# Performance work log

Hardware: AMD Instinct MI355X
Metric: run time of the kernel (lower is better)

Reference implementation:

```python
import jax, jax.numpy as jnp
import numpy as np

N = 100000      # nodes
E = 3200000     # edges (avg degree 32)
F_IN = 16       # node_features
HID = 32        # hidden_channels
OUT = 1         # out_channels


def _glorot(key, shape, fan_in):
    return (jax.random.normal(key, shape, dtype=jnp.float32) / np.sqrt(fan_in)).astype(jnp.float32)


def setup_inputs() -> dict:
    key = jax.random.key(0)
    ks = jax.random.split(key, 18)
    inp = {
        "x": jax.random.normal(ks[0], (N, F_IN), dtype=jnp.float32),
        "edge_index": jax.random.randint(ks[1], (2, E), 0, N, dtype=jnp.int64),
        "edge_weight": jax.random.uniform(ks[2], (E,), dtype=jnp.float32),
    }
    # 6 ChebConvs (K=2): x->gate convs take F_IN, h->gate convs take HID
    names_in = [("xz", F_IN), ("hz", HID), ("xr", F_IN), ("hr", HID), ("xh", F_IN), ("hh", HID)]
    for i, (nm, fin) in enumerate(names_in):
        inp[f"W_{nm}"] = _glorot(ks[3 + i], (2, fin, HID), fin)   # [K=2, in, hidden]
        inp[f"b_{nm}"] = jnp.zeros((HID,), dtype=jnp.float32)
    inp["W_lin"] = _glorot(ks[15], (HID, OUT), HID)
    inp["b_lin"] = jnp.zeros((OUT,), dtype=jnp.float32)
    return inp


def _cheb(x, W, b, src, dst, lhat_w, n):
    # ChebConv K=2, lambda_max=2: Tx0 = x, Tx1 = L_hat @ x
    tx1 = jax.ops.segment_sum(lhat_w[:, None] * x[src], dst, num_segments=n)
    return x @ W[0] + tx1 @ W[1] + b


def reference(x, edge_index, edge_weight,
              W_xz, b_xz, W_hz, b_hz,
              W_xr, b_xr, W_hr, b_hr,
              W_xh, b_xh, W_hh, b_hh,
              W_lin, b_lin):
    n = x.shape[0]
    src, dst = edge_index[0], edge_index[1]
    # scaled Laplacian edge weights: L_hat = -D^{-1/2} A D^{-1/2} (diag cancels)
    deg = jax.ops.segment_sum(edge_weight, src, num_segments=n)
    dis = jnp.where(deg > 0, jax.lax.rsqrt(jnp.maximum(deg, 1e-12)), 0.0)
    lhat_w = -dis[src] * edge_weight * dis[dst]

    H = jnp.zeros((n, W_hz.shape[1]), dtype=x.dtype)  # initial hidden state

    Z = jax.nn.sigmoid(_cheb(x, W_xz, b_xz, src, dst, lhat_w, n)
                       + _cheb(H, W_hz, b_hz, src, dst, lhat_w, n))
    R = jax.nn.sigmoid(_cheb(x, W_xr, b_xr, src, dst, lhat_w, n)
                       + _cheb(H, W_hr, b_hr, src, dst, lhat_w, n))
    H_tilde = jnp.tanh(_cheb(x, W_xh, b_xh, src, dst, lhat_w, n)
                       + _cheb(H * R, W_hh, b_hh, src, dst, lhat_w, n))
    H_new = Z * H + (1.0 - Z) * H_tilde

    h = jax.nn.relu(H_new)
    return h @ W_lin + b_lin
```

## Files before the change

### kernel.cpp

```cpp
#include <hip/hip_runtime.h>
#include <hip/hip_fp16.h>

#define N_NODES 100000
#define N_EDGES 3200000
#define F_IN 16
#define HID 32

#define NPB 128
#define NBIN 782
#define NBLK_A 512
#define EPB (N_EDGES / NBLK_A)
#define EPB2 (EPB / 2)
#define CAPB 4576
#define CAPT 9
#define SLOTS 7

typedef unsigned long long ull;
typedef float __attribute__((ext_vector_type(4))) f4v;
typedef float __attribute__((ext_vector_type(2))) f2v;

#define OFF_GCA  0
#define OFF_GCB  784
#define OFF_DIS  1568
#define OFF_XSH  101568
#define OFF_EB   901568
#define OFF_EBS  8058432

__device__ inline float2 h2f(unsigned u)
{
    __half2 h = *reinterpret_cast<__half2*>(&u);
    return __half22float2(h);
}

__global__ __launch_bounds__(512) void scatterC(
    const int* __restrict__ src, const int* __restrict__ dst,
    const float* __restrict__ w,
    int* __restrict__ gcurA, int* __restrict__ gcurB,
    uint2* __restrict__ eb, unsigned* __restrict__ ebs)
{
    __shared__ int cnt[1024];
    __shared__ int incl[1024];
    __shared__ int curs[1024];
    __shared__ int wscr[8];
    __shared__ uint2 se[EPB];

    int t = threadIdx.x, blk = blockIdx.x;
    int base = blk * EPB;
    int lane = t & 63, wid = t >> 6;

    ull sreg[SLOTS], dreg[SLOTS], wreg[SLOTS];
#pragma unroll
    for (int i = 0; i < SLOTS; ++i) {
        int k = t + (i << 9);
        if (k < EPB2) {
            sreg[i] = __builtin_nontemporal_load((const ull*)(src + base) + k);
            dreg[i] = __builtin_nontemporal_load((const ull*)(dst + base) + k);
            wreg[i] = __builtin_nontemporal_load((const ull*)(w + base) + k);
        }
    }

    cnt[2 * t] = 0; cnt[2 * t + 1] = 0;
    __syncthreads();
#pragma unroll
    for (int i = 0; i < SLOTS; ++i) {
        int k = t + (i << 9);
        if (k < EPB2) {
            atomicAdd(&cnt[(int)((unsigned)dreg[i] >> 7)], 1);
            atomicAdd(&cnt[(int)((unsigned)(dreg[i] >> 32) >> 7)], 1);
        }
    }
    __syncthreads();
    {
        int a0 = cnt[2 * t], a1 = cnt[2 * t + 1];
        int ps = a0 + a1;
        int v = ps;
#pragma unroll
        for (int off = 1; off < 64; off <<= 1) {
            int u = __shfl_up(v, off, 64);
            if (lane >= off) v += u;
        }
        if (lane == 63) wscr[wid] = v;
        __syncthreads();
        int wpre = 0;
#pragma unroll
        for (int j = 0; j < 8; ++j) wpre += (j < wid) ? wscr[j] : 0;
        int ebase = wpre + v - ps;
        incl[2 * t]     = ebase + a0;
        incl[2 * t + 1] = ebase + ps;
        curs[2 * t]     = ebase;
        curs[2 * t + 1] = ebase + a0;
    }
    __syncthreads();

    int rbA0 = 0, rbA1 = 0;
    {
        int cA0 = cnt[t];
        if (cA0) rbA0 = atomicAdd(&gcurA[t], cA0);
        if (t + 512 < NBIN) {
            int cA1 = cnt[t + 512];
            if (cA1) rbA1 = atomicAdd(&gcurA[t + 512], cA1);
        }
    }

#pragma unroll
    for (int i = 0; i < SLOTS; ++i) {
        int k = t + (i << 9);
        if (k < EPB2) {
            int s0 = (int)((unsigned)sreg[i]), s1 = (int)((unsigned)(sreg[i] >> 32));
            int d0 = (int)((unsigned)dreg[i]), d1 = (int)((unsigned)(dreg[i] >> 32));
            unsigned h0 = (unsigned)__half_as_ushort(
                              __float2half_rn(__uint_as_float((unsigned)wreg[i])));
            unsigned h1 = (unsigned)__half_as_ushort(
                              __float2half_rn(__uint_as_float((unsigned)(wreg[i] >> 32))));
            int p0 = atomicAdd(&curs[d0 >> 7], 1);
            se[p0] = make_uint2((unsigned)s0 | ((unsigned)(d0 & 127) << 17),
                                ((unsigned)(d0 >> 7) << 16) | h0);
            int p1 = atomicAdd(&curs[d1 >> 7], 1);
            se[p1] = make_uint2((unsigned)s1 | ((unsigned)(d1 & 127) << 17),
                                ((unsigned)(d1 >> 7) << 16) | h1);
        }
    }
    __syncthreads();
    curs[t] = rbA0;
    if (t + 512 < NBIN) curs[t + 512] = rbA1;
    __syncthreads();
    for (int p = t; p < EPB; p += 512) {
        uint2 v = se[p];
        int bin = (int)(v.y >> 16);
        int local = p - (incl[bin] - cnt[bin]);
        int pos = curs[bin] + local;
        if (pos < CAPB) {
            ull pv = ((ull)(v.y & 0xFFFFu) << 32) | (ull)v.x;
            __builtin_nontemporal_store(pv, (ull*)(eb + (size_t)bin * CAPB + pos));
        }
    }
    __syncthreads();

    cnt[2 * t] = 0; cnt[2 * t + 1] = 0;
    __syncthreads();
#pragma unroll
    for (int i = 0; i < SLOTS; ++i) {
        int k = t + (i << 9);
        if (k < EPB2) {
            atomicAdd(&cnt[(int)((unsigned)sreg[i] >> 7)], 1);
            atomicAdd(&cnt[(int)((unsigned)(sreg[i] >> 32) >> 7)], 1);
        }
    }
    __syncthreads();
    {
        int a0 = cnt[2 * t], a1 = cnt[2 * t + 1];
        int ps = a0 + a1;
        int v = ps;
#pragma unroll
        for (int off = 1; off < 64; off <<= 1) {
            int u = __shfl_up(v, off, 64);
            if (lane >= off) v += u;
        }
        if (lane == 63) wscr[wid] = v;
        __syncthreads();
        int wpre = 0;
#pragma unroll
        for (int j = 0; j < 8; ++j) wpre += (j < wid) ? wscr[j] : 0;
        int ebase = wpre + v - ps;
        incl[2 * t]     = ebase + a0;
        incl[2 * t + 1] = ebase + ps;
        curs[2 * t]     = ebase;
        curs[2 * t + 1] = ebase + a0;
    }
    __syncthreads();

    int rbB0 = 0, rbB1 = 0;
    {
        int cB0 = cnt[t];
        if (cB0) rbB0 = atomicAdd(&gcurB[t], cB0);
        if (t + 512 < NBIN) {
            int cB1 = cnt[t + 512];
            if (cB1) rbB1 = atomicAdd(&gcurB[t + 512], cB1);
        }
    }

#pragma unroll
    for (int i = 0; i < SLOTS; ++i) {
        int k = t + (i << 9);
        if (k < EPB2) {
            int s0 = (int)((unsigned)sreg[i]), s1 = (int)((unsigned)(sreg[i] >> 32));
            unsigned h0 = (unsigned)__half_as_ushort(
                              __float2half_rn(__uint_as_float((unsigned)wreg[i])));
            unsigned h1 = (unsigned)__half_as_ushort(
                              __float2half_rn(__uint_as_float((unsigned)(wreg[i] >> 32))));
            int p0 = atomicAdd(&curs[s0 >> 7], 1);
            se[p0] = make_uint2((unsigned)s0, h0);
            int p1 = atomicAdd(&curs[s1 >> 7], 1);
            se[p1] = make_uint2((unsigned)s1, h1);
        }
    }
    __syncthreads();
    curs[t] = rbB0;
    if (t + 512 < NBIN) curs[t + 512] = rbB1;
    __syncthreads();
    for (int p = t; p < EPB; p += 512) {
        uint2 v = se[p];
        int bin = (int)(v.x >> 7);
        int local = p - (incl[bin] - cnt[bin]);
        int pos = curs[bin] + local;
        if (pos < CAPB) {
            unsigned rec = ((v.x & 127u) << 16) | v.y;
            __builtin_nontemporal_store(rec, ebs + (size_t)bin * CAPB + pos);
        }
    }
}

__global__ __launch_bounds__(512) void degK(
    const unsigned* __restrict__ ebs, const int* __restrict__ gcurB,
    const float* __restrict__ x, float* __restrict__ dis,
    __half* __restrict__ xsh)
{
    __shared__ float sdeg[4][NPB];
    int b = blockIdx.x, t = threadIdx.x;
    int wid = t >> 6;
    if (t < NPB) { sdeg[0][t] = 0.f; sdeg[1][t] = 0.f; sdeg[2][t] = 0.f; sdeg[3][t] = 0.f; }
    __syncthreads();
    int m = gcurB[b];
    if (m > CAPB) m = CAPB;
    const unsigned* seg = ebs + (size_t)b * CAPB;
    for (int j = t; j < m; j += 512) {
        unsigned v = __builtin_nontemporal_load(seg + j);
        float wv = __half2float(__ushort_as_half((unsigned short)(v & 0xFFFF)));
        atomicAdd(&sdeg[wid & 3][v >> 16], wv);
    }
    __syncthreads();
    int n0 = b * NPB;
    if (t < NPB) {
        float dg = (sdeg[0][t] + sdeg[1][t]) + (sdeg[2][t] + sdeg[3][t]);
        float ds = (dg > 0.f) ? rsqrtf(fmaxf(dg, 1e-12f)) : 0.f;
        sdeg[0][t] = ds;
        if (n0 + t < N_NODES) dis[n0 + t] = ds;
    }
    __syncthreads();
    for (int i = t; i < NPB * 8; i += 512) {
        int node = n0 + (i >> 3);
        if (node < N_NODES) {
            float ds = sdeg[0][i >> 3];
            f2v xv = __builtin_nontemporal_load(((const f2v*)x) + node * 8 + (i & 7));
            ((__half2*)xsh)[node * 8 + (i & 7)] =
                __float22half2_rn(make_float2(xv.x * ds, xv.y * ds));
        }
    }
}

__global__ __launch_bounds__(512) void gatherNode(
    const uint2* __restrict__ eb, const int* __restrict__ gcurA,
    const float* __restrict__ dis, const __half* __restrict__ xsh,
    const float* __restrict__ x,
    const float* __restrict__ W_xz, const float* __restrict__ b_xz,
    const float* __restrict__ b_hz,
    const float* __restrict__ W_xh, const float* __restrict__ b_xh,
    const float* __restrict__ b_hh,
    const float* __restrict__ W_lin, const float* __restrict__ b_lin,
    float* __restrict__ out)
{
    __shared__ unsigned       sl[CAPB];
    __shared__ unsigned short sw[CAPB];
    __shared__ int   cnt[NPB], scn[NPB], cur[NPB];
    __shared__ int   wtot;
    __shared__ float stx[NPB * 17];
    __shared__ float sbz[HID], sbh[HID], sWl[HID];
    __shared__ float sdis[NPB];

    float* sWz = (float*)sl;
    float* sWh = (float*)sl + 2 * F_IN * HID;

    int t = threadIdx.x, b = blockIdx.x;
    int lane = t & 63, wid = t >> 6;
    int m = gcurA[b];
    if (m > CAPB) m = CAPB;
    const uint2* seg = eb + (size_t)b * CAPB;

    ull r[CAPT];
#pragma unroll
    for (int i = 0; i < CAPT; ++i) {
        int k = t + (i << 9);
        if (k < m) r[i] = __builtin_nontemporal_load((const ull*)(seg + k));
    }

    if (t < NPB) cnt[t] = 0;
    if (t < HID) {
        sbz[t] = b_xz[t] + b_hz[t];
        sbh[t] = b_xh[t] + b_hh[t];
        sWl[t] = W_lin[t];
    }
    if (t < NPB) {
        int n = b * NPB + t;
        sdis[t] = (n < N_NODES) ? dis[n] : 0.f;
    }
    __syncthreads();

#pragma unroll
    for (int i = 0; i < CAPT; ++i) {
        int k = t + (i << 9);
        if (k < m) atomicAdd(&cnt[(unsigned)r[i] >> 17], 1);
    }
    __syncthreads();
    {
        int v = (t < NPB) ? cnt[t] : 0;
#pragma unroll
        for (int off = 1; off < 64; off <<= 1) {
            int u = __shfl_up(v, off, 64);
            if (lane >= off) v += u;
        }
        if (t == 63) wtot = v;
        __syncthreads();
        if (t < NPB) {
            int vv = v + ((wid == 1) ? wtot : 0);
            scn[t] = vv;
            cur[t] = vv - cnt[t];
        }
    }
    __syncthreads();
#pragma unroll
    for (int i = 0; i < CAPT; ++i) {
        int k = t + (i << 9);
        if (k < m) {
            unsigned lo = (unsigned)r[i], hi = (unsigned)(r[i] >> 32);
            int p = atomicAdd(&cur[lo >> 17], 1);
            sl[p] = lo;
            sw[p] = (unsigned short)hi;
        }
    }
    __syncthreads();

    {
        int nloc = t >> 2;
        int h    = t & 3;
        int r1 = scn[nloc];
        int r0 = r1 - cnt[nloc];
        float dn = sdis[nloc];
        float a0 = 0.f, a1 = 0.f, a2 = 0.f, a3 = 0.f;
        int j = r0;
        for (; j + 7 < r1; j += 8) {
            unsigned e[8]; unsigned short wv[8]; uint2 p[8];
#pragma unroll
            for (int q = 0; q < 8; ++q) { e[q] = sl[j + q]; wv[q] = sw[j + q]; }
#pragma unroll
            for (int q = 0; q < 8; ++q)
                p[q] = *(const uint2*)(xsh + ((size_t)(e[q] & 0x1FFFF) << 4) + (h << 2));
#pragma unroll
            for (int q = 0; q < 8; ++q) {
                float lw = -__half2float(__ushort_as_half(wv[q])) * dn;
                float2 f0 = h2f(p[q].x), f1 = h2f(p[q].y);
                a0 = fmaf(lw, f0.x, a0); a1 = fmaf(lw, f0.y, a1);
                a2 = fmaf(lw, f1.x, a2); a3 = fmaf(lw, f1.y, a3);
            }
        }
        for (; j < r1; ++j) {
            unsigned e0 = sl[j];
            uint2 p0 = *(const uint2*)(xsh + ((size_t)(e0 & 0x1FFFF) << 4) + (h << 2));
            float lw0 = -__half2float(__ushort_as_half(sw[j])) * dn;
            float2 f;
            f = h2f(p0.x); a0 = fmaf(lw0, f.x, a0); a1 = fmaf(lw0, f.y, a1);
            f = h2f(p0.y); a2 = fmaf(lw0, f.x, a2); a3 = fmaf(lw0, f.y, a3);
        }
        float* tp = &stx[nloc * 17 + (h << 2)];
        tp[0] = a0; tp[1] = a1; tp[2] = a2; tp[3] = a3;
    }
    __syncthreads();

    for (int i = t; i < 2 * F_IN * HID; i += 512) { sWz[i] = W_xz[i]; sWh[i] = W_xh[i]; }
    __syncthreads();

    int n = b * NPB + t;
    if (t >= NPB || n >= N_NODES) return;

    float xv[F_IN], tv[F_IN];
    const f4v* xr = (const f4v*)(x + (size_t)n * F_IN);
#pragma unroll
    for (int q = 0; q < 4; ++q) {
        f4v a = __builtin_nontemporal_load(xr + q);
        xv[4 * q + 0] = a.x; xv[4 * q + 1] = a.y; xv[4 * q + 2] = a.z; xv[4 * q + 3] = a.w;
    }
#pragma unroll
    for (int k = 0; k < F_IN; ++k) tv[k] = stx[t * 17 + k];

    float acc = 0.f;
    for (int j = 0; j < HID; ++j) {
        float zp = sbz[j];
        float hp = sbh[j];
#pragma unroll
        for (int k = 0; k < F_IN; ++k) {
            zp = fmaf(xv[k], sWz[k * HID + j], zp);
            zp = fmaf(tv[k], sWz[F_IN * HID + k * HID + j], zp);
            hp = fmaf(xv[k], sWh[k * HID + j], hp);
            hp = fmaf(tv[k], sWh[F_IN * HID + k * HID + j], hp);
        }
        float z  = 1.f / (1.f + __expf(-zp));
        float ht = tanhf(hp);
        float hn = (1.f - z) * ht;
        acc = fmaf(fmaxf(hn, 0.f), sWl[j], acc);
    }
    out[n] = acc + b_lin[0];
}

extern "C" void kernel_launch(void* const* d_in, const int* in_sizes, int n_in,
                              void* d_out, int out_size, void* d_ws, size_t ws_size,
                              hipStream_t stream)
{
    const float* x     = (const float*)d_in[0];
    const int*   ei    = (const int*)d_in[1];
    const float* ew    = (const float*)d_in[2];
    const float* W_xz  = (const float*)d_in[3];
    const float* b_xz  = (const float*)d_in[4];
    const float* b_hz  = (const float*)d_in[6];
    const float* W_xh  = (const float*)d_in[11];
    const float* b_xh  = (const float*)d_in[12];
    const float* b_hh  = (const float*)d_in[14];
    const float* W_lin = (const float*)d_in[15];
    const float* b_lin = (const float*)d_in[16];
    float*       out   = (float*)d_out;

    int*      wsi = (int*)d_ws;
    float*    wsf = (float*)d_ws;

    int*      gcurA = wsi + OFF_GCA;
    int*      gcurB = wsi + OFF_GCB;
    float*    dis   = wsf + OFF_DIS;
    __half*   xsh   = (__half*)(wsi + OFF_XSH);
    uint2*    eb    = (uint2*)(wsi + OFF_EB);
    unsigned* ebs   = (unsigned*)(wsi + OFF_EBS);

    const int* src = ei;
    const int* dst = ei + N_EDGES;

    hipMemsetAsync(d_ws, 0, (size_t)OFF_DIS * 4, stream);
    scatterC<<<NBLK_A, 512, 0, stream>>>(src, dst, ew, gcurA, gcurB, eb, ebs);
    degK<<<NBIN, 512, 0, stream>>>(ebs, gcurB, x, dis, xsh);
    gatherNode<<<NBIN, 512, 0, stream>>>(eb, gcurA, dis, xsh, x,
        W_xz, b_xz, b_hz, W_xh, b_xh, b_hh, W_lin, b_lin, out);
}
```

Baseline: 227.5 us.

## Widen edge gather to 16-byte loads with edge-parity split, spread degree atomics

In the node gather, each thread now loads 8 half features (uint4) per edge instead of 4, and the four threads of a node split the edges by parity, so each edge row is fetched by two threads rather than four. Partial sums are combined with a cross-lane shuffle before the results go to shared memory. This cuts the number of gather load instructions per edge and should help use memory bandwidth better, at the cost of extra accumulator registers and a shuffle reduction. The degree kernel also spreads its LDS atomic adds over 8 per-wave copies instead of 4 to reduce contention.

```diff
diff --git a/kernel.cpp b/kernel.cpp
--- a/kernel.cpp
+++ b/kernel.cpp
@@ -215,10 +215,10 @@
     const float* __restrict__ x, float* __restrict__ dis,
     __half* __restrict__ xsh)
 {
-    __shared__ float sdeg[4][NPB];
+    __shared__ float sdeg[8][NPB];
     int b = blockIdx.x, t = threadIdx.x;
     int wid = t >> 6;
-    if (t < NPB) { sdeg[0][t] = 0.f; sdeg[1][t] = 0.f; sdeg[2][t] = 0.f; sdeg[3][t] = 0.f; }
+    for (int i = t; i < 8 * NPB; i += 512) ((float*)sdeg)[i] = 0.f;
     __syncthreads();
     int m = gcurB[b];
     if (m > CAPB) m = CAPB;
@@ -226,12 +226,13 @@
     for (int j = t; j < m; j += 512) {
         unsigned v = __builtin_nontemporal_load(seg + j);
         float wv = __half2float(__ushort_as_half((unsigned short)(v & 0xFFFF)));
-        atomicAdd(&sdeg[wid & 3][v >> 16], wv);
+        atomicAdd(&sdeg[wid][v >> 16], wv);
     }
     __syncthreads();
     int n0 = b * NPB;
     if (t < NPB) {
-        float dg = (sdeg[0][t] + sdeg[1][t]) + (sdeg[2][t] + sdeg[3][t]);
+        float dg = ((sdeg[0][t] + sdeg[1][t]) + (sdeg[2][t] + sdeg[3][t]))
+                 + ((sdeg[4][t] + sdeg[5][t]) + (sdeg[6][t] + sdeg[7][t]));
         float ds = (dg > 0.f) ? rsqrtf(fmaxf(dg, 1e-12f)) : 0.f;
         sdeg[0][t] = ds;
         if (n0 + t < N_NODES) dis[n0 + t] = ds;
@@ -332,36 +333,53 @@
     {
         int nloc = t >> 2;
         int h    = t & 3;
+        int par  = h >> 1;
+        int hf   = h & 1;
         int r1 = scn[nloc];
         int r0 = r1 - cnt[nloc];
         float dn = sdis[nloc];
         float a0 = 0.f, a1 = 0.f, a2 = 0.f, a3 = 0.f;
-        int j = r0;
-        for (; j + 7 < r1; j += 8) {
-            unsigned e[8]; unsigned short wv[8]; uint2 p[8];
-#pragma unroll
-            for (int q = 0; q < 8; ++q) { e[q] = sl[j + q]; wv[q] = sw[j + q]; }
+        float a4 = 0.f, a5 = 0.f, a6 = 0.f, a7 = 0.f;
+        int j = r0 + par;
+        for (; j + 14 < r1; j += 16) {
+            unsigned e[8]; unsigned short wv[8]; uint4 p[8];
+#pragma unroll
+            for (int q = 0; q < 8; ++q) { e[q] = sl[j + 2 * q]; wv[q] = sw[j + 2 * q]; }
 #pragma unroll
             for (int q = 0; q < 8; ++q)
-                p[q] = *(const uint2*)(xsh + ((size_t)(e[q] & 0x1FFFF) << 4) + (h << 2));
+                p[q] = *(const uint4*)(xsh + ((size_t)(e[q] & 0x1FFFF) << 4) + (hf << 3));
 #pragma unroll
             for (int q = 0; q < 8; ++q) {
                 float lw = -__half2float(__ushort_as_half(wv[q])) * dn;
                 float2 f0 = h2f(p[q].x), f1 = h2f(p[q].y);
+                float2 f2 = h2f(p[q].z), f3 = h2f(p[q].w);
                 a0 = fmaf(lw, f0.x, a0); a1 = fmaf(lw, f0.y, a1);
                 a2 = fmaf(lw, f1.x, a2); a3 = fmaf(lw, f1.y, a3);
+                a4 = fmaf(lw, f2.x, a4); a5 = fmaf(lw, f2.y, a5);
+                a6 = fmaf(lw, f3.x, a6); a7 = fmaf(lw, f3.y, a7);
             }
         }
-        for (; j < r1; ++j) {
+        for (; j < r1; j += 2) {
             unsigned e0 = sl[j];
-            uint2 p0 = *(const uint2*)(xsh + ((size_t)(e0 & 0x1FFFF) << 4) + (h << 2));
-            float lw0 = -__half2float(__ushort_as_half(sw[j])) * dn;
-            float2 f;
-            f = h2f(p0.x); a0 = fmaf(lw0, f.x, a0); a1 = fmaf(lw0, f.y, a1);
-            f = h2f(p0.y); a2 = fmaf(lw0, f.x, a2); a3 = fmaf(lw0, f.y, a3);
-        }
-        float* tp = &stx[nloc * 17 + (h << 2)];
-        tp[0] = a0; tp[1] = a1; tp[2] = a2; tp[3] = a3;
+            float lw = -__half2float(__ushort_as_half(sw[j])) * dn;
+            uint4 p0 = *(const uint4*)(xsh + ((size_t)(e0 & 0x1FFFF) << 4) + (hf << 3));
+            float2 f0 = h2f(p0.x), f1 = h2f(p0.y);
+            float2 f2 = h2f(p0.z), f3 = h2f(p0.w);
+            a0 = fmaf(lw, f0.x, a0); a1 = fmaf(lw, f0.y, a1);
+            a2 = fmaf(lw, f1.x, a2); a3 = fmaf(lw, f1.y, a3);
+            a4 = fmaf(lw, f2.x, a4); a5 = fmaf(lw, f2.y, a5);
+            a6 = fmaf(lw, f3.x, a6); a7 = fmaf(lw, f3.y, a7);
+        }
+        a0 += __shfl_xor(a0, 2, 64); a1 += __shfl_xor(a1, 2, 64);
+        a2 += __shfl_xor(a2, 2, 64); a3 += __shfl_xor(a3, 2, 64);
+        a4 += __shfl_xor(a4, 2, 64); a5 += __shfl_xor(a5, 2, 64);
+        a6 += __shfl_xor(a6, 2, 64); a7 += __shfl_xor(a7, 2, 64);
+        float w0 = par ? a4 : a0;
+        float w1 = par ? a5 : a1;
+        float w2 = par ? a6 : a2;
+        float w3 = par ? a7 : a3;
+        float* tp = &stx[nloc * 17 + (hf << 3) + (par << 2)];
+        tp[0] = w0; tp[1] = w1; tp[2] = w2; tp[3] = w3;
     }
     __syncthreads();
 
```

New measurement: 231.9 us. About the same (+1.9%).
